# Performance work log

Measured on AMD Instinct MI355X. Metric: run time of the kernel, lower is better.

## Reference

```python
import jax, jax.numpy as jnp
import numpy as np

B, K, D = 4, 2048, 512
H, DQ, DV = 8, 64, 64
ATTN_SIZE = 128  # banded local window


def setup_inputs() -> dict:
    key = jax.random.key(0)
    ks = jax.random.split(key, 11)
    s = 1.0 / np.sqrt(D)
    so = 1.0 / np.sqrt(H * DV)
    return {
        "query": jax.random.normal(ks[0], (B, K, D), jnp.float32),
        "key": jax.random.normal(ks[1], (B, K, D), jnp.float32),
        "value": jax.random.normal(ks[2], (B, K, D), jnp.float32),
        "W_q": jax.random.uniform(ks[3], (H * DQ, D), jnp.float32, -s, s),
        "b_q": jax.random.uniform(ks[4], (H * DQ,), jnp.float32, -s, s),
        "W_k": jax.random.uniform(ks[5], (H * DQ, D), jnp.float32, -s, s),
        "b_k": jax.random.uniform(ks[6], (H * DQ,), jnp.float32, -s, s),
        "W_v": jax.random.uniform(ks[7], (H * DV, D), jnp.float32, -s, s),
        "b_v": jax.random.uniform(ks[8], (H * DV,), jnp.float32, -s, s),
        "W_o": jax.random.uniform(ks[9], (D, H * DV), jnp.float32, -so, so),
        "b_o": jax.random.uniform(ks[10], (D,), jnp.float32, -so, so),
    }


def reference(query, key, value, W_q, b_q, W_k, b_k, W_v, b_v, W_o, b_o):
    Klen = query.shape[1]
    # projections; chunk(h, -1) + cat(0) in torch == per-head split of last dim
    q = (query @ W_q.T + b_q).reshape(B, Klen, H, DQ)
    k = (key @ W_k.T + b_k).reshape(B, Klen, H, DQ)
    v = (value @ W_v.T + b_v).reshape(B, Klen, H, DV)
    # NOTE: original scales by sqrt(seq_len K), not sqrt(d_k)
    scores = jnp.einsum('bihq,bjhq->bhij', q, k) / jnp.sqrt(jnp.float32(Klen))
    i = jnp.arange(Klen)[:, None]
    j = jnp.arange(Klen)[None, :]
    # banded local mask (|i-j|<=attention_size) AND causal ('subsequent')
    allowed = (jnp.abs(i - j) <= ATTN_SIZE) & (j <= i)
    scores = jnp.where(allowed, scores, jnp.float32(-jnp.inf))
    probs = jax.nn.softmax(scores, axis=-1)
    attn = jnp.einsum('bhij,bjhv->bihv', probs, v).reshape(B, Klen, H * DV)
    return attn @ W_o.T + b_o
```

## Files before the change

### kernel.cpp

```cpp
#include <hip/hip_runtime.h>
#include <hip/hip_bf16.h>
#include <stdint.h>

#define B_ 4
#define K_ 2048
#define D_ 512
#define H_ 8
#define ATTN_ 128
#define M_ (B_ * K_)

typedef __attribute__((ext_vector_type(4))) float f32x4;
typedef __attribute__((ext_vector_type(8))) short bf16x8;
typedef __attribute__((ext_vector_type(8))) unsigned short u16x8;
typedef __attribute__((ext_vector_type(2))) unsigned int u32x2;
typedef __attribute__((ext_vector_type(4))) unsigned int u32x4;

__device__ __forceinline__ unsigned short f2bf(float f) {
    union { float f; unsigned int i; } x; x.f = f;
    unsigned int r = x.i + 0x7fffu + ((x.i >> 16) & 1u);
    return (unsigned short)(r >> 16);
}
__device__ __forceinline__ float bf2f(unsigned short u) {
    union { unsigned int i; float f; } x; x.i = ((unsigned int)u) << 16; return x.f;
}
__device__ __forceinline__ void gload_lds16(const unsigned short* g, unsigned short* l) {
    __builtin_amdgcn_global_load_lds(
        (const __attribute__((address_space(1))) void*)g,
        (__attribute__((address_space(3))) void*)l, 16, 0, 0);
}
__device__ __forceinline__ unsigned lds_addr(const void* p) {
    return (unsigned)(unsigned long long)
        (const __attribute__((address_space(3))) void*)p;
}

struct Cvt { const float* s; unsigned short* d; int n8; };
struct CvtA { Cvt c[4]; };

__global__ __launch_bounds__(256)
void cvt_multi(CvtA a) {
    const Cvt c = a.c[blockIdx.y];
    const float4* s4 = (const float4*)c.s;
    u16x8* d8 = (u16x8*)c.d;
    for (int g = blockIdx.x * 256 + threadIdx.x; g < c.n8; g += gridDim.x * 256) {
        float4 f0 = s4[2 * g], f1 = s4[2 * g + 1];
        u16x8 o;
        o[0] = f2bf(f0.x); o[1] = f2bf(f0.y); o[2] = f2bf(f0.z); o[3] = f2bf(f0.w);
        o[4] = f2bf(f1.x); o[5] = f2bf(f1.y); o[6] = f2bf(f1.z); o[7] = f2bf(f1.w);
        d8[g] = o;
    }
}

struct GArgs {
    const void* A[3];
    const unsigned short* Wt[3];
    const float* bias[3];
    void* C[3];
};

template<bool A_FP32>
__global__ __launch_bounds__(256, 3)
void gemm128(GArgs args)
{
    __shared__ unsigned short As[128 * 64];
    __shared__ unsigned short Bs[128 * 64];

    const int id = blockIdx.x;
    const int lg = (id & 7) * (gridDim.x >> 3) + (id >> 3);
    const int g  = lg >> 2;
    const int nt = lg & 3;
    const int z  = A_FP32 ? (g >> 6) : 0;
    const int mt = A_FP32 ? (g & 63) : g;
    const int bm = mt * 128;
    const int bn = nt * 128;

    const void* Az = args.A[z];
    const unsigned short* Wz = args.Wt[z];
    const float* biz = args.bias[z];
    void* Cz = args.C[z];

    const int tid = threadIdx.x;
    const int w   = tid >> 6;
    const int l   = tid & 63;
    const int lr  = l & 15;
    const int lhi = l >> 4;
    const int wm  = (w >> 1) * 64;
    const int wn  = (w & 1) * 64;

    f32x4 acc[4][4];
    #pragma unroll
    for (int m = 0; m < 4; ++m)
        #pragma unroll
        for (int n = 0; n < 4; ++n) acc[m][n] = (f32x4){0.f, 0.f, 0.f, 0.f};

    float4 fa[4][2];

    auto loadA_f32 = [&](int t) {
        #pragma unroll
        for (int q = 0; q < 4; ++q) {
            const int cid = q * 256 + tid;
            const int r = cid >> 3;
            const int c = (cid & 7) ^ (r & 7);
            const float* src = (const float*)Az + (size_t)(bm + r) * D_ + t * 64 + c * 8;
            fa[q][0] = *(const float4*)src;
            fa[q][1] = *(const float4*)(src + 4);
        }
    };
    auto writeA_f32 = [&]() {
        #pragma unroll
        for (int q = 0; q < 4; ++q) {
            const int cid = q * 256 + tid;
            u16x8 o;
            o[0] = f2bf(fa[q][0].x); o[1] = f2bf(fa[q][0].y);
            o[2] = f2bf(fa[q][0].z); o[3] = f2bf(fa[q][0].w);
            o[4] = f2bf(fa[q][1].x); o[5] = f2bf(fa[q][1].y);
            o[6] = f2bf(fa[q][1].z); o[7] = f2bf(fa[q][1].w);
            *(u16x8*)&As[cid * 8] = o;
        }
    };
    auto stageA_b16 = [&](int t) {
        #pragma unroll
        for (int it = 0; it < 4; ++it) {
            const int cg  = it * 4 + w;
            const int cid = cg * 64 + l;
            const int r = cid >> 3;
            const int c = (cid & 7) ^ (r & 7);
            gload_lds16((const unsigned short*)Az + (size_t)(bm + r) * D_ + t * 64 + c * 8,
                        &As[cg * 512]);
        }
    };
    auto stageB = [&](int t) {
        #pragma unroll
        for (int it = 0; it < 4; ++it) {
            const int cg  = it * 4 + w;
            const int cid = cg * 64 + l;
            const int r = cid >> 3;
            const int c = (cid & 7) ^ (r & 7);
            gload_lds16(Wz + (size_t)(bn + r) * D_ + t * 64 + c * 8,
                        &Bs[cg * 512]);
        }
    };

    if (A_FP32) { loadA_f32(0); writeA_f32(); }
    else        { stageA_b16(0); }
    stageB(0);
    __syncthreads();

    for (int t = 0; t < 8; ++t) {
        if (A_FP32 && t < 7) loadA_f32(t + 1);
        #pragma unroll
        for (int kk = 0; kk < 2; ++kk) {
            bf16x8 af[4], bfr[4];
            #pragma unroll
            for (int fm = 0; fm < 4; ++fm) {
                const int row = wm + fm * 16 + lr;
                const int sl  = (kk * 4 + lhi) ^ (row & 7);
                af[fm] = *(const bf16x8*)&As[row * 64 + sl * 8];
            }
            #pragma unroll
            for (int fn = 0; fn < 4; ++fn) {
                const int row = wn + fn * 16 + lr;
                const int sl  = (kk * 4 + lhi) ^ (row & 7);
                bfr[fn] = *(const bf16x8*)&Bs[row * 64 + sl * 8];
            }
            #pragma unroll
            for (int fm = 0; fm < 4; ++fm)
                #pragma unroll
                for (int fn = 0; fn < 4; ++fn)
                    acc[fm][fn] = __builtin_amdgcn_mfma_f32_16x16x32_bf16(
                        af[fm], bfr[fn], acc[fm][fn], 0, 0, 0);
        }
        __syncthreads();
        if (t < 7) {
            if (A_FP32) writeA_f32();
            else        stageA_b16(t + 1);
            stageB(t + 1);
            __syncthreads();
        }
    }

    float bv[4];
    #pragma unroll
    for (int fn = 0; fn < 4; ++fn) bv[fn] = biz[bn + wn + fn * 16 + lr];

    #pragma unroll
    for (int fm = 0; fm < 4; ++fm)
        #pragma unroll
        for (int fn = 0; fn < 4; ++fn)
            #pragma unroll
            for (int rr = 0; rr < 4; ++rr) {
                const int row = bm + wm + fm * 16 + lhi * 4 + rr;
                const int col = bn + wn + fn * 16 + lr;
                const float val = acc[fm][fn][rr] + bv[fn];
                if (A_FP32)
                    ((unsigned short*)Cz)[(size_t)row * 512 + col] = f2bf(val);
                else
                    ((float*)Cz)[(size_t)row * 512 + col] = val;
            }
}

__global__ __launch_bounds__(256)
void attn_mfma(const unsigned short* __restrict__ qb,
               const unsigned short* __restrict__ kb,
               const unsigned short* __restrict__ vb,
               unsigned short* __restrict__ ob)
{
    __shared__ unsigned short Ksh[192 * 64];
    __shared__ unsigned short Vsh[4 * 192 * 16];
    __shared__ unsigned short Psh[4 * 16 * 200];

    const int flat = blockIdx.x + 32 * (blockIdx.y + 8 * blockIdx.z);
    const int lg   = (flat & 7) * 128 + (flat >> 3);
    const int tile = lg & 31;
    const int h    = (lg >> 5) & 7;
    const int b    = lg >> 8;

    const int i0 = tile * 64;
    const int j0 = i0 - 128;
    const int tid = threadIdx.x;
    const int w   = tid >> 6;
    const int l   = tid & 63;
    const int lr  = l & 15;
    const int lhi = l >> 4;
    const float scale = 0.0220970869120796f;

    const size_t hbase = ((size_t)b * K_) * 512 + (size_t)h * 64;
    const unsigned short* kh = kb + hbase;
    const unsigned short* vh = vb + hbase;
    const unsigned short* qh = qb + hbase;
    unsigned short* oh = ob + hbase;

    #pragma unroll
    for (int it = 0; it < 6; ++it) {
        const int cg  = it * 4 + w;
        const int cid = cg * 64 + l;
        const int r = cid >> 3, c = cid & 7;
        const int cs = c ^ (r & 7);
        int j = j0 + r; if (j < 0) j = 0;
        gload_lds16(kh + (size_t)j * 512 + cs * 8, &Ksh[cg * 64 * 8]);
    }
    #pragma unroll
    for (int it = 0; it < 6; ++it) {
        const int cg  = it * 4 + w;
        const int cid = cg * 64 + l;
        const int blk = cid / 384;
        const int rem = cid - blk * 384;
        const int prow = rem >> 1, hf = rem & 1;
        const int a = prow >> 2, bb = prow & 3;
        const int k = (a < 24) ? (8 * a + bb) : (8 * (a - 24) + 4 + bb);
        int j = j0 + k; if (j < 0) j = 0;
        gload_lds16(vh + (size_t)j * 512 + blk * 16 + hf * 8, &Vsh[cg * 64 * 8]);
    }

    bf16x8 qa[2];
    {
        const unsigned short* qrow = qh + (size_t)(i0 + 16 * w + lr) * 512;
        qa[0] = *(const bf16x8*)(qrow + lhi * 8);
        qa[1] = *(const bf16x8*)(qrow + 32 + lhi * 8);
    }
    __syncthreads();

    const int jcbase = w & ~1;
    f32x4 sacc[10];
    #pragma unroll
    for (int jc = 0; jc < 10; ++jc) sacc[jc] = (f32x4){0.f, 0.f, 0.f, 0.f};

    __builtin_amdgcn_s_setprio(1);
    #pragma unroll
    for (int kk = 0; kk < 2; ++kk) {
        const int ch = (kk * 4 + lhi) ^ (lr & 7);
        #pragma unroll
        for (int jc = 0; jc < 10; ++jc) {
            const int row = (jcbase + jc) * 16 + lr;
            bf16x8 kf = *(const bf16x8*)&Ksh[row * 64 + ch * 8];
            sacc[jc] = __builtin_amdgcn_mfma_f32_16x16x32_bf16(
                qa[kk], kf, sacc[jc], 0, 0, 0);
        }
    }
    __builtin_amdgcn_s_setprio(0);

    unsigned short* myP = &Psh[w * 3200];
    const int lo0 = 128 - i0;
    float lsum[4] = {0.f, 0.f, 0.f, 0.f};
    #pragma unroll
    for (int jc = 0; jc < 10; ++jc) {
        const int jcol = (jcbase + jc) * 16 + lr;
        #pragma unroll
        for (int rr = 0; rr < 4; ++rr) {
            const int iloc = 16 * w + 4 * lhi + rr;
            const bool ok = (jcol >= iloc) && (jcol <= iloc + ATTN_) && (jcol >= lo0);
            const float p = ok ? __expf(fminf(sacc[jc][rr] * scale, 80.f)) : 0.f;
            lsum[rr] += p;
            myP[(4 * lhi + rr) * 200 + jcol] = f2bf(p);
        }
    }
    #pragma unroll
    for (int rr = 0; rr < 4; ++rr) {
        float s = lsum[rr];
        s += __shfl_xor(s, 1, 16);
        s += __shfl_xor(s, 2, 16);
        s += __shfl_xor(s, 4, 16);
        s += __shfl_xor(s, 8, 16);
        lsum[rr] = s;
    }

    const int kcbase = w >> 1;
    f32x4 oacc[4];
    #pragma unroll
    for (int fn = 0; fn < 4; ++fn) oacc[fn] = (f32x4){0.f, 0.f, 0.f, 0.f};
    const unsigned vbase = lds_addr(&Vsh[0]) + (unsigned)(l * 8);

    for (int kc5 = 0; kc5 < 5; ++kc5) {
        const int kc = kcbase + kc5;
        bf16x8 pa = *(const bf16x8*)&myP[lr * 200 + kc * 32 + lhi * 8];
        u32x2 vlo[4], vhi[4];
        #pragma unroll
        for (int fn = 0; fn < 4; ++fn) {
            const unsigned addr = vbase + (unsigned)((fn * 3072 + kc * 256) * 2);
            asm volatile("ds_read_b64_tr_b16 %0, %1" : "=v"(vlo[fn]) : "v"(addr));
            asm volatile("ds_read_b64_tr_b16 %0, %1 offset:3072"
                         : "=v"(vhi[fn]) : "v"(addr));
        }
        asm volatile("s_waitcnt lgkmcnt(0)" ::: "memory");
        __builtin_amdgcn_sched_barrier(0);
        __builtin_amdgcn_s_setprio(1);
        #pragma unroll
        for (int fn = 0; fn < 4; ++fn) {
            union { u32x2 h[2]; bf16x8 v; } u;
            u.h[0] = vlo[fn]; u.h[1] = vhi[fn];
            oacc[fn] = __builtin_amdgcn_mfma_f32_16x16x32_bf16(
                pa, u.v, oacc[fn], 0, 0, 0);
        }
        __builtin_amdgcn_s_setprio(0);
    }

    float inv[4];
    #pragma unroll
    for (int rr = 0; rr < 4; ++rr) inv[rr] = 1.f / lsum[rr];
    #pragma unroll
    for (int fn = 0; fn < 4; ++fn)
        #pragma unroll
        for (int rr = 0; rr < 4; ++rr) {
            const int row = i0 + 16 * w + 4 * lhi + rr;
            oh[(size_t)row * 512 + fn * 16 + lr] = f2bf(oacc[fn][rr] * inv[rr]);
        }
}

extern "C" void kernel_launch(void* const* d_in, const int* in_sizes, int n_in,
                              void* d_out, int out_size, void* d_ws, size_t ws_size,
                              hipStream_t stream)
{
    const float* query = (const float*)d_in[0];
    const float* key   = (const float*)d_in[1];
    const float* value = (const float*)d_in[2];
    const float* W_q   = (const float*)d_in[3];
    const float* b_q   = (const float*)d_in[4];
    const float* W_k   = (const float*)d_in[5];
    const float* b_k   = (const float*)d_in[6];
    const float* W_v   = (const float*)d_in[7];
    const float* b_v   = (const float*)d_in[8];
    const float* W_o   = (const float*)d_in[9];
    const float* b_o   = (const float*)d_in[10];
    float* out = (float*)d_out;

    const size_t NX = (size_t)M_ * 512;
    const size_t NW = 512 * 512;
    unsigned short* wqb = (unsigned short*)d_ws;
    unsigned short* wkb = wqb + NW;
    unsigned short* wvb = wkb + NW;
    unsigned short* wob = wvb + NW;
    unsigned short* qp  = wob + NW;
    unsigned short* kp  = qp + NX;
    unsigned short* vp  = kp + NX;
    unsigned short* ap  = vp + NX;

    const int NW8 = (int)(NW / 8);

    CvtA a;
    a.c[0] = { W_q, wqb, NW8 };
    a.c[1] = { W_k, wkb, NW8 };
    a.c[2] = { W_v, wvb, NW8 };
    a.c[3] = { W_o, wob, NW8 };
    cvt_multi<<<dim3(32, 4), 256, 0, stream>>>(a);

    GArgs qa;
    qa.A[0] = query; qa.A[1] = key; qa.A[2] = value;
    qa.Wt[0] = wqb;  qa.Wt[1] = wkb; qa.Wt[2] = wvb;
    qa.bias[0] = b_q; qa.bias[1] = b_k; qa.bias[2] = b_v;
    qa.C[0] = qp; qa.C[1] = kp; qa.C[2] = vp;
    gemm128<true><<<768, 256, 0, stream>>>(qa);

    attn_mfma<<<dim3(32, 8, 4), 256, 0, stream>>>(qp, kp, vp, ap);

    GArgs oa;
    oa.A[0] = ap; oa.A[1] = ap; oa.A[2] = ap;
    oa.Wt[0] = wob; oa.Wt[1] = wob; oa.Wt[2] = wob;
    oa.bias[0] = b_o; oa.bias[1] = b_o; oa.bias[2] = b_o;
    oa.C[0] = out; oa.C[1] = out; oa.C[2] = out;
    gemm128<false><<<256, 256, 0, stream>>>(oa);
}
```

Before: 59.89 us.

## Double-buffer LDS tiles in QKV and output GEMMs with async prefetch

Splits the templated GEMM into a QKV kernel and an output-projection kernel. Both now double-buffer shared-memory tiles so the next K-step's global-to-LDS loads are issued before the current step's MFMAs, which is meant to hide load latency. Both also raise wave priority around the MFMA section. The cost is more shared memory per block, which may lower occupancy; the output GEMM declares launch bounds of 2 blocks per CU.

```diff
diff --git a/kernel.cpp b/kernel.cpp
--- a/kernel.cpp
+++ b/kernel.cpp
@@ -13,7 +13,6 @@
 typedef __attribute__((ext_vector_type(8))) short bf16x8;
 typedef __attribute__((ext_vector_type(8))) unsigned short u16x8;
 typedef __attribute__((ext_vector_type(2))) unsigned int u32x2;
-typedef __attribute__((ext_vector_type(4))) unsigned int u32x4;
 
 __device__ __forceinline__ unsigned short f2bf(float f) {
     union { float f; unsigned int i; } x; x.f = f;
@@ -57,26 +56,25 @@
     void* C[3];
 };
 
-template<bool A_FP32>
 __global__ __launch_bounds__(256, 3)
-void gemm128(GArgs args)
+void gemm_qkv128(GArgs args)
 {
     __shared__ unsigned short As[128 * 64];
-    __shared__ unsigned short Bs[128 * 64];
+    __shared__ unsigned short Bs[2][128 * 64];
 
     const int id = blockIdx.x;
     const int lg = (id & 7) * (gridDim.x >> 3) + (id >> 3);
     const int g  = lg >> 2;
     const int nt = lg & 3;
-    const int z  = A_FP32 ? (g >> 6) : 0;
-    const int mt = A_FP32 ? (g & 63) : g;
+    const int z  = g >> 6;
+    const int mt = g & 63;
     const int bm = mt * 128;
     const int bn = nt * 128;
 
-    const void* Az = args.A[z];
+    const float* Az = (const float*)args.A[z];
     const unsigned short* Wz = args.Wt[z];
     const float* biz = args.bias[z];
-    void* Cz = args.C[z];
+    unsigned short* Cz = (unsigned short*)args.C[z];
 
     const int tid = threadIdx.x;
     const int w   = tid >> 6;
@@ -100,7 +98,7 @@
             const int cid = q * 256 + tid;
             const int r = cid >> 3;
             const int c = (cid & 7) ^ (r & 7);
-            const float* src = (const float*)Az + (size_t)(bm + r) * D_ + t * 64 + c * 8;
+            const float* src = Az + (size_t)(bm + r) * D_ + t * 64 + c * 8;
             fa[q][0] = *(const float4*)src;
             fa[q][1] = *(const float4*)(src + 4);
         }
@@ -117,18 +115,7 @@
             *(u16x8*)&As[cid * 8] = o;
         }
     };
-    auto stageA_b16 = [&](int t) {
-        #pragma unroll
-        for (int it = 0; it < 4; ++it) {
-            const int cg  = it * 4 + w;
-            const int cid = cg * 64 + l;
-            const int r = cid >> 3;
-            const int c = (cid & 7) ^ (r & 7);
-            gload_lds16((const unsigned short*)Az + (size_t)(bm + r) * D_ + t * 64 + c * 8,
-                        &As[cg * 512]);
-        }
-    };
-    auto stageB = [&](int t) {
+    auto stageB = [&](int buf, int t) {
         #pragma unroll
         for (int it = 0; it < 4; ++it) {
             const int cg  = it * 4 + w;
@@ -136,17 +123,21 @@
             const int r = cid >> 3;
             const int c = (cid & 7) ^ (r & 7);
             gload_lds16(Wz + (size_t)(bn + r) * D_ + t * 64 + c * 8,
-                        &Bs[cg * 512]);
+                        &Bs[buf][cg * 512]);
         }
     };
 
-    if (A_FP32) { loadA_f32(0); writeA_f32(); }
-    else        { stageA_b16(0); }
-    stageB(0);
+    loadA_f32(0);
+    writeA_f32();
+    stageB(0, 0);
     __syncthreads();
 
     for (int t = 0; t < 8; ++t) {
-        if (A_FP32 && t < 7) loadA_f32(t + 1);
+        if (t < 7) {
+            loadA_f32(t + 1);
+            stageB((t + 1) & 1, t + 1);
+        }
+        __builtin_amdgcn_s_setprio(1);
         #pragma unroll
         for (int kk = 0; kk < 2; ++kk) {
             bf16x8 af[4], bfr[4];
@@ -160,7 +151,7 @@
             for (int fn = 0; fn < 4; ++fn) {
                 const int row = wn + fn * 16 + lr;
                 const int sl  = (kk * 4 + lhi) ^ (row & 7);
-                bfr[fn] = *(const bf16x8*)&Bs[row * 64 + sl * 8];
+                bfr[fn] = *(const bf16x8*)&Bs[t & 1][row * 64 + sl * 8];
             }
             #pragma unroll
             for (int fm = 0; fm < 4; ++fm)
@@ -169,11 +160,10 @@
                     acc[fm][fn] = __builtin_amdgcn_mfma_f32_16x16x32_bf16(
                         af[fm], bfr[fn], acc[fm][fn], 0, 0, 0);
         }
-        __syncthreads();
+        __builtin_amdgcn_s_setprio(0);
         if (t < 7) {
-            if (A_FP32) writeA_f32();
-            else        stageA_b16(t + 1);
-            stageB(t + 1);
+            __syncthreads();
+            writeA_f32();
             __syncthreads();
         }
     }
@@ -190,11 +180,108 @@
             for (int rr = 0; rr < 4; ++rr) {
                 const int row = bm + wm + fm * 16 + lhi * 4 + rr;
                 const int col = bn + wn + fn * 16 + lr;
-                const float val = acc[fm][fn][rr] + bv[fn];
-                if (A_FP32)
-                    ((unsigned short*)Cz)[(size_t)row * 512 + col] = f2bf(val);
-                else
-                    ((float*)Cz)[(size_t)row * 512 + col] = val;
+                Cz[(size_t)row * 512 + col] = f2bf(acc[fm][fn][rr] + bv[fn]);
+            }
+}
+
+__global__ __launch_bounds__(256, 2)
+void gemm_o128(const unsigned short* __restrict__ A,
+               const unsigned short* __restrict__ W,
+               const float* __restrict__ bias,
+               float* __restrict__ C)
+{
+    __shared__ unsigned short As[2][128 * 64];
+    __shared__ unsigned short Bs[2][128 * 64];
+
+    const int id = blockIdx.x;
+    const int lg = (id & 7) * (gridDim.x >> 3) + (id >> 3);
+    const int mt = lg >> 2;
+    const int nt = lg & 3;
+    const int bm = mt * 128;
+    const int bn = nt * 128;
+
+    const int tid = threadIdx.x;
+    const int w   = tid >> 6;
+    const int l   = tid & 63;
+    const int lr  = l & 15;
+    const int lhi = l >> 4;
+    const int wm  = (w >> 1) * 64;
+    const int wn  = (w & 1) * 64;
+
+    f32x4 acc[4][4];
+    #pragma unroll
+    for (int m = 0; m < 4; ++m)
+        #pragma unroll
+        for (int n = 0; n < 4; ++n) acc[m][n] = (f32x4){0.f, 0.f, 0.f, 0.f};
+
+    auto stage = [&](int buf, int t) {
+        #pragma unroll
+        for (int it = 0; it < 4; ++it) {
+            const int cg  = it * 4 + w;
+            const int cid = cg * 64 + l;
+            const int r = cid >> 3;
+            const int c = (cid & 7) ^ (r & 7);
+            gload_lds16(A + (size_t)(bm + r) * D_ + t * 64 + c * 8,
+                        &As[buf][cg * 512]);
+        }
+        #pragma unroll
+        for (int it = 0; it < 4; ++it) {
+            const int cg  = it * 4 + w;
+            const int cid = cg * 64 + l;
+            const int r = cid >> 3;
+            const int c = (cid & 7) ^ (r & 7);
+            gload_lds16(W + (size_t)(bn + r) * D_ + t * 64 + c * 8,
+                        &Bs[buf][cg * 512]);
+        }
+    };
+
+    stage(0, 0);
+    __syncthreads();
+
+    int buf = 0;
+    for (int t = 0; t < 8; ++t) {
+        if (t < 7) stage(buf ^ 1, t + 1);
+        __builtin_amdgcn_s_setprio(1);
+        #pragma unroll
+        for (int kk = 0; kk < 2; ++kk) {
+            bf16x8 af[4], bfr[4];
+            #pragma unroll
+            for (int fm = 0; fm < 4; ++fm) {
+                const int row = wm + fm * 16 + lr;
+                const int sl  = (kk * 4 + lhi) ^ (row & 7);
+                af[fm] = *(const bf16x8*)&As[buf][row * 64 + sl * 8];
+            }
+            #pragma unroll
+            for (int fn = 0; fn < 4; ++fn) {
+                const int row = wn + fn * 16 + lr;
+                const int sl  = (kk * 4 + lhi) ^ (row & 7);
+                bfr[fn] = *(const bf16x8*)&Bs[buf][row * 64 + sl * 8];
+            }
+            #pragma unroll
+            for (int fm = 0; fm < 4; ++fm)
+                #pragma unroll
+                for (int fn = 0; fn < 4; ++fn)
+                    acc[fm][fn] = __builtin_amdgcn_mfma_f32_16x16x32_bf16(
+                        af[fm], bfr[fn], acc[fm][fn], 0, 0, 0);
+        }
+        __builtin_amdgcn_s_setprio(0);
+        __syncthreads();
+        buf ^= 1;
+    }
+
+    float bv[4];
+    #pragma unroll
+    for (int fn = 0; fn < 4; ++fn) bv[fn] = bias[bn + wn + fn * 16 + lr];
+
+    #pragma unroll
+    for (int fm = 0; fm < 4; ++fm)
+        #pragma unroll
+        for (int fn = 0; fn < 4; ++fn)
+            #pragma unroll
+            for (int rr = 0; rr < 4; ++rr) {
+                const int row = bm + wm + fm * 16 + lhi * 4 + rr;
+                const int col = bn + wn + fn * 16 + lr;
+                C[(size_t)row * 512 + col] = acc[fm][fn][rr] + bv[fn];
             }
 }
 
@@ -387,14 +474,9 @@
     qa.Wt[0] = wqb;  qa.Wt[1] = wkb; qa.Wt[2] = wvb;
     qa.bias[0] = b_q; qa.bias[1] = b_k; qa.bias[2] = b_v;
     qa.C[0] = qp; qa.C[1] = kp; qa.C[2] = vp;
-    gemm128<true><<<768, 256, 0, stream>>>(qa);
+    gemm_qkv128<<<768, 256, 0, stream>>>(qa);
 
     attn_mfma<<<dim3(32, 8, 4), 256, 0, stream>>>(qp, kp, vp, ap);
 
-    GArgs oa;
-    oa.A[0] = ap; oa.A[1] = ap; oa.A[2] = ap;
-    oa.Wt[0] = wob; oa.Wt[1] = wob; oa.Wt[2] = wob;
-    oa.bias[0] = b_o; oa.bias[1] = b_o; oa.bias[2] = b_o;
-    oa.C[0] = out; oa.C[1] = out; oa.C[2] = out;
-    gemm128<false><<<256, 256, 0, stream>>>(oa);
-}
+    gemm_o128<<<256, 256, 0, stream>>>(ap, wob, b_o, out);
+}
```

After: 56.29 us. -6.0%, faster.
